# Kernel tuning notes

Measured on AMD Instinct MI355X. Metric: run time of the kernel, lower is better.

The kernel has to match this reference:

```python
import jax, jax.numpy as jnp
import numpy as np

TEMPERATURE = 1.0
K = 30
N_CELLS = 200000
LATENT = 256
BATCH = 8192

def setup_inputs() -> dict:
    key = jax.random.key(0)
    k1, k2, k3, k4 = jax.random.split(key, 4)
    z_all = jax.random.normal(k1, (N_CELLS, LATENT), dtype=jnp.float32)
    pre_knn_indices = jax.random.randint(k2, (N_CELLS, K), 0, N_CELLS, dtype=jnp.int64)
    cell_indices = jax.random.randint(k3, (BATCH,), 0, N_CELLS, dtype=jnp.int64)
    neg_indices = jax.random.randint(k4, (BATCH, K), 0, N_CELLS, dtype=jnp.int64)
    return {"z_all": z_all, "pre_knn_indices": pre_knn_indices,
            "cell_indices": cell_indices, "neg_indices": neg_indices}

def reference(z_all, pre_knn_indices, cell_indices, neg_indices):
    # z_all: (N, D); pre_knn_indices: (N, K); cell_indices: (B,); neg_indices: (B, K)
    z_i = z_all[cell_indices]                       # (B, D)
    nn_idx = pre_knn_indices[cell_indices]          # (B, K)
    z_nn = z_all[nn_idx]                            # (B, K, D)
    z_neg = z_all[neg_indices]                      # (B, K, D)
    d_nn = jnp.linalg.norm(z_nn - z_i[:, None, :], axis=-1)    # (B, K)
    d_neg = jnp.linalg.norm(z_neg - z_i[:, None, :], axis=-1)  # (B, K)
    all_dist = jnp.concatenate([d_nn, d_neg], axis=1)          # (B, 2K)
    soft_prob = jax.nn.softmax(-all_dist / TEMPERATURE, axis=1)
    soft_np = soft_prob[:, :K].sum(axis=1)                     # (B,)
    losses = -jnp.log(soft_np + 1e-8)
    return losses.mean()
```

## Files before the change

### kernel.cpp

```cpp
#include <hip/hip_runtime.h>
#include <math.h>

#define BATCH  8192
#define KNEI   30
#define LATENT 256
#define NDIST  60
#define ROWS_PER_WAVE 15

__global__ __launch_bounds__(256) void softnp_dist_kernel(
    const float* __restrict__ z_all,
    const int* __restrict__ knn,
    const int* __restrict__ cell,
    const int* __restrict__ neg,
    float* __restrict__ losses)
{
    const int b    = blockIdx.x;
    const int tid  = threadIdx.x;
    const int wave = tid >> 6;
    const int lane = tid & 63;

    __shared__ float dist[NDIST + 4];

    const int ci = cell[b];

    const float4 zv = reinterpret_cast<const float4*>(z_all + (size_t)ci * LATENT)[lane];

    int idx[ROWS_PER_WAVE];
    #pragma unroll
    for (int j = 0; j < ROWS_PER_WAVE; ++j) {
        const int k = wave + 4 * j;
        idx[j] = (k < KNEI) ? knn[(size_t)ci * KNEI + k]
                            : neg[(size_t)b * KNEI + (k - KNEI)];
    }

    float4 v[ROWS_PER_WAVE];
    #pragma unroll
    for (int j = 0; j < ROWS_PER_WAVE; ++j)
        v[j] = reinterpret_cast<const float4*>(z_all + (size_t)idx[j] * LATENT)[lane];

    float s[ROWS_PER_WAVE];
    #pragma unroll
    for (int j = 0; j < ROWS_PER_WAVE; ++j) {
        const float dx = v[j].x - zv.x;
        const float dy = v[j].y - zv.y;
        const float dz = v[j].z - zv.z;
        const float dw = v[j].w - zv.w;
        s[j] = dx * dx + dy * dy + dz * dz + dw * dw;
    }

    #pragma unroll
    for (int off = 32; off > 0; off >>= 1) {
        #pragma unroll
        for (int j = 0; j < ROWS_PER_WAVE; ++j)
            s[j] += __shfl_xor(s[j], off, 64);
    }

    if (lane == 0) {
        #pragma unroll
        for (int j = 0; j < ROWS_PER_WAVE; ++j)
            dist[wave + 4 * j] = sqrtf(s[j]);
    }
    __syncthreads();

    if (wave == 0) {
        const float sc = (lane < NDIST) ? -dist[lane] : -INFINITY;

        float m = sc;
        #pragma unroll
        for (int off = 32; off > 0; off >>= 1)
            m = fmaxf(m, __shfl_xor(m, off, 64));

        const float e = (lane < NDIST) ? expf(sc - m) : 0.0f;
        float tot = e;
        float top = (lane < KNEI) ? e : 0.0f;
        #pragma unroll
        for (int off = 32; off > 0; off >>= 1) {
            tot += __shfl_xor(tot, off, 64);
            top += __shfl_xor(top, off, 64);
        }

        if (lane == 0)
            losses[b] = -logf(top / tot + 1e-8f);
    }
}

__global__ __launch_bounds__(1024) void softnp_reduce_kernel(
    const float* __restrict__ losses, float* __restrict__ out)
{
    const int tid  = threadIdx.x;
    const int wave = tid >> 6;
    const int lane = tid & 63;

    float s = 0.0f;
    for (int i = tid; i < BATCH; i += 1024)
        s += losses[i];

    #pragma unroll
    for (int off = 32; off > 0; off >>= 1)
        s += __shfl_xor(s, off, 64);

    __shared__ float buf[16];
    if (lane == 0) buf[wave] = s;
    __syncthreads();

    if (tid == 0) {
        float t = 0.0f;
        #pragma unroll
        for (int i = 0; i < 16; ++i) t += buf[i];
        out[0] = t / (float)BATCH;
    }
}

extern "C" void kernel_launch(void* const* d_in, const int* in_sizes, int n_in,
                              void* d_out, int out_size, void* d_ws, size_t ws_size,
                              hipStream_t stream) {
    const float* z_all = (const float*)d_in[0];
    const int*   knn   = (const int*)d_in[1];
    const int*   cell  = (const int*)d_in[2];
    const int*   neg   = (const int*)d_in[3];
    float* out    = (float*)d_out;
    float* losses = (float*)d_ws;

    softnp_dist_kernel<<<BATCH, 256, 0, stream>>>(z_all, knn, cell, neg, losses);
    softnp_reduce_kernel<<<1, 1024, 0, stream>>>(losses, out);
}
```

Baseline: 82.75 us.

## Assign one batch row per wavefront and drop shared-memory block sync

Each wavefront now handles a whole batch element: it gathers all 60 rows in chunks of 10, reduces the distances with shuffles, and computes the softmax loss locally, with no shared memory or __syncthreads. Index loads are coalesced, one lane per neighbor, and broadcast with __shfl. This removes the block barrier and the serial softmax tail in which only wave 0 worked. The cost is fewer loads in flight per wave (10 per chunk instead of 15) and extra shuffle work per wave.

```diff
diff --git a/kernel.cpp b/kernel.cpp
--- a/kernel.cpp
+++ b/kernel.cpp
@@ -5,7 +5,8 @@
 #define KNEI   30
 #define LATENT 256
 #define NDIST  60
-#define ROWS_PER_WAVE 15
+#define CHUNK  10
+#define NCHUNK (NDIST / CHUNK)
 
 __global__ __launch_bounds__(256) void softnp_dist_kernel(
     const float* __restrict__ z_all,
@@ -14,74 +15,75 @@
     const int* __restrict__ neg,
     float* __restrict__ losses)
 {
-    const int b    = blockIdx.x;
     const int tid  = threadIdx.x;
     const int wave = tid >> 6;
     const int lane = tid & 63;
-
-    __shared__ float dist[NDIST + 4];
+    const int b    = blockIdx.x * 4 + wave;
 
     const int ci = cell[b];
 
     const float4 zv = reinterpret_cast<const float4*>(z_all + (size_t)ci * LATENT)[lane];
 
-    int idx[ROWS_PER_WAVE];
+    int myidx = 0;
+    if (lane < KNEI)
+        myidx = knn[(size_t)ci * KNEI + lane];
+    else if (lane >= 32 && lane < 32 + KNEI)
+        myidx = neg[(size_t)b * KNEI + (lane - 32)];
+
+    float dreg = -INFINITY;
+
     #pragma unroll
-    for (int j = 0; j < ROWS_PER_WAVE; ++j) {
-        const int k = wave + 4 * j;
-        idx[j] = (k < KNEI) ? knn[(size_t)ci * KNEI + k]
-                            : neg[(size_t)b * KNEI + (k - KNEI)];
+    for (int c = 0; c < NCHUNK; ++c) {
+        float4 v[CHUNK];
+        #pragma unroll
+        for (int j = 0; j < CHUNK; ++j) {
+            const int k   = c * CHUNK + j;
+            const int src = (k < KNEI) ? k : k + 2;
+            const int idx = __shfl(myidx, src, 64);
+            v[j] = reinterpret_cast<const float4*>(z_all + (size_t)idx * LATENT)[lane];
+        }
+
+        float s[CHUNK];
+        #pragma unroll
+        for (int j = 0; j < CHUNK; ++j) {
+            const float dx = v[j].x - zv.x;
+            const float dy = v[j].y - zv.y;
+            const float dz = v[j].z - zv.z;
+            const float dw = v[j].w - zv.w;
+            s[j] = dx * dx + dy * dy + dz * dz + dw * dw;
+        }
+
+        #pragma unroll
+        for (int off = 32; off > 0; off >>= 1) {
+            #pragma unroll
+            for (int j = 0; j < CHUNK; ++j)
+                s[j] += __shfl_xor(s[j], off, 64);
+        }
+
+        #pragma unroll
+        for (int j = 0; j < CHUNK; ++j) {
+            const int k   = c * CHUNK + j;
+            const int src = (k < KNEI) ? k : k + 2;
+            if (lane == src) dreg = -sqrtf(s[j]);
+        }
     }
 
-    float4 v[ROWS_PER_WAVE];
+    float m = dreg;
     #pragma unroll
-    for (int j = 0; j < ROWS_PER_WAVE; ++j)
-        v[j] = reinterpret_cast<const float4*>(z_all + (size_t)idx[j] * LATENT)[lane];
+    for (int off = 32; off > 0; off >>= 1)
+        m = fmaxf(m, __shfl_xor(m, off, 64));
 
-    float s[ROWS_PER_WAVE];
+    const float e   = expf(dreg - m);
+    float tot = e;
+    float top = (lane < KNEI) ? e : 0.0f;
     #pragma unroll
-    for (int j = 0; j < ROWS_PER_WAVE; ++j) {
-        const float dx = v[j].x - zv.x;
-        const float dy = v[j].y - zv.y;
-        const float dz = v[j].z - zv.z;
-        const float dw = v[j].w - zv.w;
-        s[j] = dx * dx + dy * dy + dz * dz + dw * dw;
+    for (int off = 32; off > 0; off >>= 1) {
+        tot += __shfl_xor(tot, off, 64);
+        top += __shfl_xor(top, off, 64);
     }
 
-    #pragma unroll
-    for (int off = 32; off > 0; off >>= 1) {
-        #pragma unroll
-        for (int j = 0; j < ROWS_PER_WAVE; ++j)
-            s[j] += __shfl_xor(s[j], off, 64);
-    }
-
-    if (lane == 0) {
-        #pragma unroll
-        for (int j = 0; j < ROWS_PER_WAVE; ++j)
-            dist[wave + 4 * j] = sqrtf(s[j]);
-    }
-    __syncthreads();
-
-    if (wave == 0) {
-        const float sc = (lane < NDIST) ? -dist[lane] : -INFINITY;
-
-        float m = sc;
-        #pragma unroll
-        for (int off = 32; off > 0; off >>= 1)
-            m = fmaxf(m, __shfl_xor(m, off, 64));
-
-        const float e = (lane < NDIST) ? expf(sc - m) : 0.0f;
-        float tot = e;
-        float top = (lane < KNEI) ? e : 0.0f;
-        #pragma unroll
-        for (int off = 32; off > 0; off >>= 1) {
-            tot += __shfl_xor(tot, off, 64);
-            top += __shfl_xor(top, off, 64);
-        }
-
-        if (lane == 0)
-            losses[b] = -logf(top / tot + 1e-8f);
-    }
+    if (lane == 0)
+        losses[b] = -logf(top / tot + 1e-8f);
 }
 
 __global__ __launch_bounds__(1024) void softnp_reduce_kernel(
@@ -121,6 +123,6 @@
     float* out    = (float*)d_out;
     float* losses = (float*)d_ws;
 
-    softnp_dist_kernel<<<BATCH, 256, 0, stream>>>(z_all, knn, cell, neg, losses);
+    softnp_dist_kernel<<<BATCH / 4, 256, 0, stream>>>(z_all, knn, cell, neg, losses);
     softnp_reduce_kernel<<<1, 1024, 0, stream>>>(losses, out);
 }
```

Result: no change. 83.52 us (+0.9%).
